# Kernel optimization log

Hardware: AMD Instinct MI355X
Metric: run time of the kernel (lower is better)

Reference implementation:

```python
import jax, jax.numpy as jnp
import numpy as np

N = 50000   # nodes
E = 800000  # edges (before self-loops)


def _gcn_conv(X, W, b, src, dst, dinv, n):
    # PyG GCNConv: out[i] = sum_j norm_ij * (X W)[j] + b, norm_ij = d_i^-1/2 d_j^-1/2
    h = X @ W                                   # [N, d_out]
    norm = dinv[src] * dinv[dst]                # [E+N]
    msg = h[src] * norm[:, None]                # gather + scale
    return jax.ops.segment_sum(msg, dst, num_segments=n) + b


def setup_inputs() -> dict:
    key = jax.random.key(0)
    k1, k2, k3, k4 = jax.random.split(key, 4)
    X = jax.random.normal(k1, (N, 128), dtype=jnp.float32)
    edge_index = jax.random.randint(k2, (2, E), 0, N, dtype=jnp.int64)
    W1 = jax.random.normal(k3, (128, 128), dtype=jnp.float32) * (1.0 / np.sqrt(128))
    b1 = jnp.zeros((128,), jnp.float32)
    W2 = jax.random.normal(k4, (128, 64), dtype=jnp.float32) * (1.0 / np.sqrt(128))
    b2 = jnp.zeros((64,), jnp.float32)
    return {"X": X, "edge_index": edge_index, "W1": W1, "b1": b1, "W2": W2, "b2": b2}


def reference(X, edge_index, W1, b1, W2, b2):
    n = X.shape[0]
    loops = jnp.arange(n, dtype=edge_index.dtype)
    src = jnp.concatenate([edge_index[0], loops])   # A + I
    dst = jnp.concatenate([edge_index[1], loops])
    deg = jax.ops.segment_sum(jnp.ones(src.shape[0], X.dtype), dst, num_segments=n)
    dinv = jnp.where(deg > 0, jax.lax.rsqrt(deg), 0.0)

    h = _gcn_conv(X, W1, b1, src, dst, dinv, n)                     # gcn1
    h = jax.nn.relu(_gcn_conv(h, W1, b1, src, dst, dinv, n))        # gcn1 again (as in source), relu
    # dropout: eval mode (identity)
    logits = _gcn_conv(h, W2, b2, src, dst, dinv, n)                # gcn2
    return jax.nn.log_softmax(logits, axis=1)
```

## Files before the change

### kernel.cpp

```cpp
#include <hip/hip_runtime.h>
#include <hip/hip_fp16.h>
#include <type_traits>

typedef _Float16 f16x8 __attribute__((ext_vector_type(8)));
typedef float    f32x4 __attribute__((ext_vector_type(4)));

__device__ inline unsigned int pack2(float a, float b) {
    __half2 h = __floats2half2_rn(a, b);
    return *(unsigned int*)&h;
}
__device__ inline float2 unpack2(unsigned int u) {
    __half2 h = *(__half2*)&u;
    return __half22float2(h);
}

#define MAXB 8192


__global__ void zero_kernel(int* __restrict__ p, int len) {
    int i = blockIdx.x * blockDim.x + threadIdx.x;
    if (i < len) p[i] = 0;
}

__global__ __launch_bounds__(256) void bucket_scatter_kernel(
    const int* __restrict__ src, const int* __restrict__ dst, int E, int nbuck,
    int* __restrict__ bcursor, unsigned int* __restrict__ staging) {
    __shared__ int hist[256];
    __shared__ int base[256];
    const int t = threadIdx.x;
    const int chunk = (E + gridDim.x - 1) / gridDim.x;
    const int e0 = blockIdx.x * chunk;
    const int e1 = min(E, e0 + chunk);
    for (int i = t; i < nbuck; i += 256) hist[i] = 0;
    __syncthreads();
    for (int e = e0 + t; e < e1; e += 256)
        atomicAdd(&hist[((unsigned)dst[e]) >> 8], 1);
    __syncthreads();
    for (int i = t; i < nbuck; i += 256) {
        int c = hist[i];
        base[i] = (c > 0) ? atomicAdd(&bcursor[i], c) : 0;
        hist[i] = 0;
    }
    __syncthreads();
    for (int e = e0 + t; e < e1; e += 256) {
        int d = dst[e];
        int b = ((unsigned)d) >> 8;
        int off = atomicAdd(&hist[b], 1);
        staging[(size_t)b * MAXB + base[b] + off] =
            (unsigned)src[e] | ((unsigned)(d & 255) << 16);
    }
}

__global__ __launch_bounds__(256) void bucket_hist_kernel(
    const unsigned int* __restrict__ staging, const int* __restrict__ bcursor,
    int n, int* __restrict__ counts, float* __restrict__ dinv) {
    __shared__ int hist[256];
    const int b = blockIdx.x, t = threadIdx.x;
    hist[t] = 0;
    __syncthreads();
    const int cnt = bcursor[b];
    const unsigned int* rec = staging + (size_t)b * MAXB;
    for (int i = t; i < cnt; i += 256) atomicAdd(&hist[(rec[i] >> 16) & 255], 1);
    __syncthreads();
    int node = (b << 8) + t;
    if (node < n) {
        int c = hist[t];
        counts[node] = c;
        dinv[node]   = rsqrtf(1.0f + (float)c);
    }
}

__global__ __launch_bounds__(256) void scan_bexcl_kernel(const int* __restrict__ bcursor,
                                                         int* __restrict__ bexcl, int nb) {
    __shared__ int s[256];
    int t = threadIdx.x;
    int v = (t < nb) ? bcursor[t] : 0;
    s[t] = v;
    __syncthreads();
    for (int off = 1; off < 256; off <<= 1) {
        int u = (t >= off) ? s[t - off] : 0;
        __syncthreads();
        s[t] += u;
        __syncthreads();
    }
    if (t < nb) bexcl[t] = s[t] - v;
}

__global__ __launch_bounds__(256) void scan_write_kernel(const int* __restrict__ counts,
                                                         const int* __restrict__ blockoff, int n,
                                                         int* __restrict__ rowptr) {
    __shared__ int s[256];
    int t = threadIdx.x;
    int i = blockIdx.x * 256 + t;
    int v = (i < n) ? counts[i] : 0;
    s[t] = v;
    __syncthreads();
    for (int off = 1; off < 256; off <<= 1) {
        int u = (t >= off) ? s[t - off] : 0;
        __syncthreads();
        s[t] += u;
        __syncthreads();
    }
    int excl = blockoff[blockIdx.x] + s[t] - v;
    if (i < n) {
        rowptr[i] = excl;
        if (i == n - 1) rowptr[n] = excl + v;
    }
}

__global__ __launch_bounds__(256) void bucket_place_kernel(
    const unsigned int* __restrict__ staging, const int* __restrict__ bcursor,
    const int* __restrict__ rowptr, int n, unsigned short* __restrict__ edges) {
    __shared__ int lcur[256];
    const int b = blockIdx.x, t = threadIdx.x;
    int node = (b << 8) + t;
    lcur[t] = rowptr[min(node, n)];
    __syncthreads();
    const int cnt = bcursor[b];
    const unsigned int* rec = staging + (size_t)b * MAXB;
    for (int i = t; i < cnt; i += 256) {
        unsigned r = rec[i];
        int dl = (r >> 16) & 255;
        int p  = atomicAdd(&lcur[dl], 1);
        edges[p] = (unsigned short)(r & 0xffffu);
    }
}

template <int DOUT, typename TIN>
__global__ __launch_bounds__(256) void gemm_mfma(const TIN* __restrict__ A,
                                                 const float* __restrict__ W,
                                                 const float* __restrict__ dinv,
                                                 __half* __restrict__ C, int n) {
    constexpr int NF = DOUT / 16;
    __shared__ __align__(16) unsigned char wlds[DOUT * 256];

    const int t = threadIdx.x;
    for (int p = t; p < 64 * DOUT; p += 256) {
        int nn = p % DOUT;
        int k  = (p / DOUT) * 2;
        float w0 = W[(size_t)k * DOUT + nn];
        float w1 = W[(size_t)(k + 1) * DOUT + nn];
        int byte = (nn * 256 + k * 2) ^ ((nn & 7) << 4);
        *(unsigned int*)(wlds + byte) = pack2(w0, w1);
    }
    __syncthreads();

    const int w  = t >> 6;
    const int l  = t & 63;
    const int m  = (blockIdx.x * 4 + w) * 16 + (l & 15);
    const int kq = l >> 4;
    const bool valid = (m < n);

    f32x4 acc[NF];
#pragma unroll
    for (int i = 0; i < NF; ++i) acc[i] = (f32x4){0.f, 0.f, 0.f, 0.f};

#pragma unroll
    for (int ks = 0; ks < 4; ++ks) {
        const int k0 = ks * 32 + kq * 8;
        f16x8 af = {0, 0, 0, 0, 0, 0, 0, 0};
        if (valid) {
            if constexpr (std::is_same<TIN, float>::value) {
                const float4 x0 = *(const float4*)&A[(size_t)m * 128 + k0];
                const float4 x1 = *(const float4*)&A[(size_t)m * 128 + k0 + 4];
                af[0] = (_Float16)x0.x; af[1] = (_Float16)x0.y;
                af[2] = (_Float16)x0.z; af[3] = (_Float16)x0.w;
                af[4] = (_Float16)x1.x; af[5] = (_Float16)x1.y;
                af[6] = (_Float16)x1.z; af[7] = (_Float16)x1.w;
            } else {
                af = *(const f16x8*)&A[(size_t)m * 128 + k0];
            }
        }
#pragma unroll
        for (int nf = 0; nf < NF; ++nf) {
            int nn = nf * 16 + (l & 15);
            int byte = (nn * 256 + k0 * 2) ^ ((nn & 7) << 4);
            f16x8 bf = *(const f16x8*)(wlds + byte);
            acc[nf] = __builtin_amdgcn_mfma_f32_16x16x32_f16(bf, af, acc[nf], 0, 0, 0);
        }
    }

    if (valid) {
        const float di = dinv[m];
#pragma unroll
        for (int nf = 0; nf < NF; ++nf) {
            uint2 o;
            o.x = pack2(di * acc[nf][0], di * acc[nf][1]);
            o.y = pack2(di * acc[nf][2], di * acc[nf][3]);
            *(uint2*)&C[(size_t)m * DOUT + nf * 16 + kq * 4] = o;
        }
    }
}

template <int DOUT, bool RELU, bool LSM, typename TOUT>
__global__ __launch_bounds__(256) void agg_kernel(const __half* __restrict__ H,
                                                  const int* __restrict__ rowptr,
                                                  const unsigned short* __restrict__ edges,
                                                  const float* __restrict__ dinv,
                                                  const float* __restrict__ bias,
                                                  TOUT* __restrict__ out, int n) {
    constexpr int LPR = DOUT / 8;
    constexpr int EPW = 64 / LPR;
    const int t    = threadIdx.x;
    const int row  = blockIdx.x * 4 + (t >> 6);
    if (row >= n) return;
    const int lane = t & 63;
    const int sub  = lane / LPR;
    const int fl   = lane % LPR;

    const uint4* Hv = (const uint4*)H;

    float a[8] = {0.f, 0.f, 0.f, 0.f, 0.f, 0.f, 0.f, 0.f};
    auto accum = [&](uint4 h) {
        float2 f;
        f = unpack2(h.x); a[0] += f.x; a[1] += f.y;
        f = unpack2(h.y); a[2] += f.x; a[3] += f.y;
        f = unpack2(h.z); a[4] += f.x; a[5] += f.y;
        f = unpack2(h.w); a[6] += f.x; a[7] += f.y;
    };

    if (sub == 0) accum(Hv[(size_t)row * LPR + fl]);

    int j        = rowptr[row] + sub;
    const int je = rowptr[row + 1];
    for (; j + EPW < je; j += 2 * EPW) {
        int s0 = edges[j];
        int s1 = edges[j + EPW];
        uint4 h0 = Hv[(size_t)s0 * LPR + fl];
        uint4 h1 = Hv[(size_t)s1 * LPR + fl];
        accum(h0);
        accum(h1);
    }
    if (j < je) accum(Hv[(size_t)edges[j] * LPR + fl]);

#pragma unroll
    for (int off = LPR; off < 64; off <<= 1) {
#pragma unroll
        for (int i = 0; i < 8; ++i) a[i] += __shfl_xor(a[i], off, 64);
    }

    const float di = dinv[row];
    const float4 b0 = ((const float4*)bias)[fl * 2];
    const float4 b1 = ((const float4*)bias)[fl * 2 + 1];
    a[0] = b0.x + di * a[0]; a[1] = b0.y + di * a[1];
    a[2] = b0.z + di * a[2]; a[3] = b0.w + di * a[3];
    a[4] = b1.x + di * a[4]; a[5] = b1.y + di * a[5];
    a[6] = b1.z + di * a[6]; a[7] = b1.w + di * a[7];

    if (RELU) {
#pragma unroll
        for (int i = 0; i < 8; ++i) a[i] = fmaxf(a[i], 0.f);
    }

    if constexpr (LSM) {
        float m8 = a[0];
#pragma unroll
        for (int i = 1; i < 8; ++i) m8 = fmaxf(m8, a[i]);
#pragma unroll
        for (int off = 1; off < LPR; off <<= 1) m8 = fmaxf(m8, __shfl_xor(m8, off, LPR));
        float s = 0.f;
#pragma unroll
        for (int i = 0; i < 8; ++i) s += expf(a[i] - m8);
#pragma unroll
        for (int off = 1; off < LPR; off <<= 1) s += __shfl_xor(s, off, LPR);
        float ls = m8 + logf(s);
        if (sub == 0) {
            float* op = (float*)out + (size_t)row * DOUT + fl * 8;
            *(float4*)op       = make_float4(a[0] - ls, a[1] - ls, a[2] - ls, a[3] - ls);
            *(float4*)(op + 4) = make_float4(a[4] - ls, a[5] - ls, a[6] - ls, a[7] - ls);
        }
    } else {
        if (sub == 0) {
            uint4 o;
            o.x = pack2(a[0], a[1]);
            o.y = pack2(a[2], a[3]);
            o.z = pack2(a[4], a[5]);
            o.w = pack2(a[6], a[7]);
            *(uint4*)&((__half*)out)[(size_t)row * DOUT + fl * 8] = o;
        }
    }
}


extern "C" void kernel_launch(void* const* d_in, const int* in_sizes, int n_in,
                              void* d_out, int out_size, void* d_ws, size_t ws_size,
                              hipStream_t stream) {
    const float* X  = (const float*)d_in[0];
    const int*   ei = (const int*)d_in[1];
    const float* W1 = (const float*)d_in[2];
    const float* b1 = (const float*)d_in[3];
    const float* W2 = (const float*)d_in[4];
    const float* b2 = (const float*)d_in[5];

    const int n = in_sizes[0] / 128;
    const int E = in_sizes[1] / 2;
    const int* src = ei;
    const int* dst = ei + E;
    const int nbuck = (n + 255) >> 8;

    char* ws = (char*)d_ws;
    size_t off = 0;
    auto alloc = [&](size_t bytes) -> void* {
        void* p = ws + off;
        off = (off + bytes + 255) & ~(size_t)255;
        return p;
    };
    float*          dinv    = (float*)alloc((size_t)n * 4);
    int*            counts  = (int*)  alloc((size_t)n * 4);
    int*            rowptr  = (int*)  alloc((size_t)(n + 1) * 4);
    int*            bcursor = (int*)  alloc((size_t)nbuck * 4);
    int*            bexcl   = (int*)  alloc((size_t)nbuck * 4);
    unsigned int*   staging = (unsigned int*)alloc((size_t)nbuck * MAXB * 4);
    unsigned short* edges   = (unsigned short*)alloc((size_t)E * 2);
    __half*         P       = (__half*)alloc((size_t)n * 128 * 2);
    __half*         Q       = (__half*)alloc((size_t)n * 128 * 2);

    const int nb = (n + 255) / 256;

    zero_kernel<<<1, 256, 0, stream>>>(bcursor, nbuck);
    bucket_scatter_kernel<<<392, 256, 0, stream>>>(src, dst, E, nbuck, bcursor, staging);
    bucket_hist_kernel<<<nbuck, 256, 0, stream>>>(staging, bcursor, n, counts, dinv);
    scan_bexcl_kernel<<<1, 256, 0, stream>>>(bcursor, bexcl, nbuck);
    scan_write_kernel<<<nb, 256, 0, stream>>>(counts, bexcl, n, rowptr);
    bucket_place_kernel<<<nbuck, 256, 0, stream>>>(staging, bcursor, rowptr, n, edges);

    const int gb = (n + 63) / 64;
    const int ab = (n + 3) / 4;

    gemm_mfma<128, float><<<gb, 256, 0, stream>>>(X, W1, dinv, P, n);
    agg_kernel<128, false, false, __half><<<ab, 256, 0, stream>>>(
        P, rowptr, edges, dinv, b1, Q, n);

    gemm_mfma<128, __half><<<gb, 256, 0, stream>>>(Q, W1, dinv, P, n);
    agg_kernel<128, true, false, __half><<<ab, 256, 0, stream>>>(
        P, rowptr, edges, dinv, b1, Q, n);

    gemm_mfma<64, __half><<<gb, 256, 0, stream>>>(Q, W2, dinv, P, n);
    agg_kernel<64, false, true, float><<<ab, 256, 0, stream>>>(
        P, rowptr, edges, dinv, b2, (float*)d_out, n);
}
```

Before: 193.7 us.

## Sort rows by degree and aggregate one row per lane group

Result: faster. 189.4 us (-2.2%).

```diff
diff --git a/kernel.cpp b/kernel.cpp
--- a/kernel.cpp
+++ b/kernel.cpp
@@ -53,10 +53,13 @@
 
 __global__ __launch_bounds__(256) void bucket_hist_kernel(
     const unsigned int* __restrict__ staging, const int* __restrict__ bcursor,
-    int n, int* __restrict__ counts, float* __restrict__ dinv) {
+    int n, int* __restrict__ counts, float* __restrict__ dinv,
+    int* __restrict__ deghist) {
     __shared__ int hist[256];
+    __shared__ int dh[256];
     const int b = blockIdx.x, t = threadIdx.x;
     hist[t] = 0;
+    dh[t] = 0;
     __syncthreads();
     const int cnt = bcursor[b];
     const unsigned int* rec = staging + (size_t)b * MAXB;
@@ -67,14 +70,17 @@
         int c = hist[t];
         counts[node] = c;
         dinv[node]   = rsqrtf(1.0f + (float)c);
-    }
-}
-
-__global__ __launch_bounds__(256) void scan_bexcl_kernel(const int* __restrict__ bcursor,
-                                                         int* __restrict__ bexcl, int nb) {
+        atomicAdd(&dh[min(c, 255)], 1);
+    }
+    __syncthreads();
+    if (dh[t] > 0) atomicAdd(&deghist[t], dh[t]);
+}
+
+__global__ __launch_bounds__(256) void scan_small_kernel(const int* __restrict__ in,
+                                                         int* __restrict__ out, int nb) {
     __shared__ int s[256];
     int t = threadIdx.x;
-    int v = (t < nb) ? bcursor[t] : 0;
+    int v = (t < nb) ? in[t] : 0;
     s[t] = v;
     __syncthreads();
     for (int off = 1; off < 256; off <<= 1) {
@@ -83,7 +89,7 @@
         s[t] += u;
         __syncthreads();
     }
-    if (t < nb) bexcl[t] = s[t] - v;
+    if (t < nb) out[t] = s[t] - v;
 }
 
 __global__ __launch_bounds__(256) void scan_write_kernel(const int* __restrict__ counts,
@@ -105,6 +111,32 @@
     if (i < n) {
         rowptr[i] = excl;
         if (i == n - 1) rowptr[n] = excl + v;
+    }
+}
+
+__global__ __launch_bounds__(256) void perm_kernel(const int* __restrict__ counts,
+                                                   int* __restrict__ degoff, int n,
+                                                   int* __restrict__ perm) {
+    __shared__ int dh[256];
+    __shared__ int dbase[256];
+    const int t = threadIdx.x;
+    const int i = blockIdx.x * 256 + t;
+    dh[t] = 0;
+    __syncthreads();
+    int c = 0;
+    const bool v = (i < n);
+    if (v) {
+        c = min(counts[i], 255);
+        atomicAdd(&dh[c], 1);
+    }
+    __syncthreads();
+    int h = dh[t];
+    dbase[t] = (h > 0) ? atomicAdd(&degoff[t], h) : 0;
+    dh[t] = 0;
+    __syncthreads();
+    if (v) {
+        int off = atomicAdd(&dh[c], 1);
+        perm[dbase[c] + off] = i;
     }
 }
 
@@ -196,21 +228,28 @@
 __global__ __launch_bounds__(256) void agg_kernel(const __half* __restrict__ H,
                                                   const int* __restrict__ rowptr,
                                                   const unsigned short* __restrict__ edges,
+                                                  const int* __restrict__ perm,
                                                   const float* __restrict__ dinv,
                                                   const float* __restrict__ bias,
                                                   TOUT* __restrict__ out, int n) {
     constexpr int LPR = DOUT / 8;
-    constexpr int EPW = 64 / LPR;
-    const int t    = threadIdx.x;
-    const int row  = blockIdx.x * 4 + (t >> 6);
-    if (row >= n) return;
-    const int lane = t & 63;
-    const int sub  = lane / LPR;
-    const int fl   = lane % LPR;
+    constexpr int RPB = 256 / LPR;
+    const int rid  = blockIdx.x * RPB + threadIdx.x / LPR;
+    const int lane = threadIdx.x % LPR;
+    if (rid >= n) return;
+    const int row = perm[rid];
 
     const uint4* Hv = (const uint4*)H;
 
-    float a[8] = {0.f, 0.f, 0.f, 0.f, 0.f, 0.f, 0.f, 0.f};
+    float a[8];
+    {
+        uint4 h = Hv[(size_t)row * LPR + lane];
+        float2 f;
+        f = unpack2(h.x); a[0] = f.x; a[1] = f.y;
+        f = unpack2(h.y); a[2] = f.x; a[3] = f.y;
+        f = unpack2(h.z); a[4] = f.x; a[5] = f.y;
+        f = unpack2(h.w); a[6] = f.x; a[7] = f.y;
+    }
     auto accum = [&](uint4 h) {
         float2 f;
         f = unpack2(h.x); a[0] += f.x; a[1] += f.y;
@@ -219,29 +258,21 @@
         f = unpack2(h.w); a[6] += f.x; a[7] += f.y;
     };
 
-    if (sub == 0) accum(Hv[(size_t)row * LPR + fl]);
-
-    int j        = rowptr[row] + sub;
+    int j        = rowptr[row];
     const int je = rowptr[row + 1];
-    for (; j + EPW < je; j += 2 * EPW) {
+    for (; j + 1 < je; j += 2) {
         int s0 = edges[j];
-        int s1 = edges[j + EPW];
-        uint4 h0 = Hv[(size_t)s0 * LPR + fl];
-        uint4 h1 = Hv[(size_t)s1 * LPR + fl];
+        int s1 = edges[j + 1];
+        uint4 h0 = Hv[(size_t)s0 * LPR + lane];
+        uint4 h1 = Hv[(size_t)s1 * LPR + lane];
         accum(h0);
         accum(h1);
     }
-    if (j < je) accum(Hv[(size_t)edges[j] * LPR + fl]);
-
-#pragma unroll
-    for (int off = LPR; off < 64; off <<= 1) {
-#pragma unroll
-        for (int i = 0; i < 8; ++i) a[i] += __shfl_xor(a[i], off, 64);
-    }
+    if (j < je) accum(Hv[(size_t)edges[j] * LPR + lane]);
 
     const float di = dinv[row];
-    const float4 b0 = ((const float4*)bias)[fl * 2];
-    const float4 b1 = ((const float4*)bias)[fl * 2 + 1];
+    const float4 b0 = ((const float4*)bias)[lane * 2];
+    const float4 b1 = ((const float4*)bias)[lane * 2 + 1];
     a[0] = b0.x + di * a[0]; a[1] = b0.y + di * a[1];
     a[2] = b0.z + di * a[2]; a[3] = b0.w + di * a[3];
     a[4] = b1.x + di * a[4]; a[5] = b1.y + di * a[5];
@@ -264,20 +295,16 @@
 #pragma unroll
         for (int off = 1; off < LPR; off <<= 1) s += __shfl_xor(s, off, LPR);
         float ls = m8 + logf(s);
-        if (sub == 0) {
-            float* op = (float*)out + (size_t)row * DOUT + fl * 8;
-            *(float4*)op       = make_float4(a[0] - ls, a[1] - ls, a[2] - ls, a[3] - ls);
-            *(float4*)(op + 4) = make_float4(a[4] - ls, a[5] - ls, a[6] - ls, a[7] - ls);
-        }
+        float* op = (float*)out + (size_t)row * DOUT + lane * 8;
+        *(float4*)op       = make_float4(a[0] - ls, a[1] - ls, a[2] - ls, a[3] - ls);
+        *(float4*)(op + 4) = make_float4(a[4] - ls, a[5] - ls, a[6] - ls, a[7] - ls);
     } else {
-        if (sub == 0) {
-            uint4 o;
-            o.x = pack2(a[0], a[1]);
-            o.y = pack2(a[2], a[3]);
-            o.z = pack2(a[4], a[5]);
-            o.w = pack2(a[6], a[7]);
-            *(uint4*)&((__half*)out)[(size_t)row * DOUT + fl * 8] = o;
-        }
+        uint4 o;
+        o.x = pack2(a[0], a[1]);
+        o.y = pack2(a[2], a[3]);
+        o.z = pack2(a[4], a[5]);
+        o.w = pack2(a[6], a[7]);
+        *(uint4*)&((__half*)out)[(size_t)row * DOUT + lane * 8] = o;
     }
 }
 
@@ -305,11 +332,15 @@
         off = (off + bytes + 255) & ~(size_t)255;
         return p;
     };
+    int*            zbuf    = (int*)  alloc((size_t)(nbuck + 256) * 4);
+    int*            bcursor = zbuf;
+    int*            deghist = zbuf + nbuck;
     float*          dinv    = (float*)alloc((size_t)n * 4);
     int*            counts  = (int*)  alloc((size_t)n * 4);
     int*            rowptr  = (int*)  alloc((size_t)(n + 1) * 4);
-    int*            bcursor = (int*)  alloc((size_t)nbuck * 4);
     int*            bexcl   = (int*)  alloc((size_t)nbuck * 4);
+    int*            degoff  = (int*)  alloc(256 * 4);
+    int*            perm    = (int*)  alloc((size_t)n * 4);
     unsigned int*   staging = (unsigned int*)alloc((size_t)nbuck * MAXB * 4);
     unsigned short* edges   = (unsigned short*)alloc((size_t)E * 2);
     __half*         P       = (__half*)alloc((size_t)n * 128 * 2);
@@ -317,25 +348,28 @@
 
     const int nb = (n + 255) / 256;
 
-    zero_kernel<<<1, 256, 0, stream>>>(bcursor, nbuck);
+    zero_kernel<<<(nbuck + 256 + 255) / 256, 256, 0, stream>>>(zbuf, nbuck + 256);
     bucket_scatter_kernel<<<392, 256, 0, stream>>>(src, dst, E, nbuck, bcursor, staging);
-    bucket_hist_kernel<<<nbuck, 256, 0, stream>>>(staging, bcursor, n, counts, dinv);
-    scan_bexcl_kernel<<<1, 256, 0, stream>>>(bcursor, bexcl, nbuck);
+    bucket_hist_kernel<<<nbuck, 256, 0, stream>>>(staging, bcursor, n, counts, dinv, deghist);
+    scan_small_kernel<<<1, 256, 0, stream>>>(bcursor, bexcl, nbuck);
+    scan_small_kernel<<<1, 256, 0, stream>>>(deghist, degoff, 256);
     scan_write_kernel<<<nb, 256, 0, stream>>>(counts, bexcl, n, rowptr);
+    perm_kernel<<<nb, 256, 0, stream>>>(counts, degoff, n, perm);
     bucket_place_kernel<<<nbuck, 256, 0, stream>>>(staging, bcursor, rowptr, n, edges);
 
     const int gb = (n + 63) / 64;
-    const int ab = (n + 3) / 4;
+    const int ab16 = (n + 15) / 16;
+    const int ab32 = (n + 31) / 32;
 
     gemm_mfma<128, float><<<gb, 256, 0, stream>>>(X, W1, dinv, P, n);
-    agg_kernel<128, false, false, __half><<<ab, 256, 0, stream>>>(
-        P, rowptr, edges, dinv, b1, Q, n);
+    agg_kernel<128, false, false, __half><<<ab16, 256, 0, stream>>>(
+        P, rowptr, edges, perm, dinv, b1, Q, n);
 
     gemm_mfma<128, __half><<<gb, 256, 0, stream>>>(Q, W1, dinv, P, n);
-    agg_kernel<128, true, false, __half><<<ab, 256, 0, stream>>>(
-        P, rowptr, edges, dinv, b1, Q, n);
+    agg_kernel<128, true, false, __half><<<ab16, 256, 0, stream>>>(
+        P, rowptr, edges, perm, dinv, b1, Q, n);
 
     gemm_mfma<64, __half><<<gb, 256, 0, stream>>>(Q, W2, dinv, P, n);
-    agg_kernel<64, false, true, float><<<ab, 256, 0, stream>>>(
-        P, rowptr, edges, dinv, b2, (float*)d_out, n);
-}
+    agg_kernel<64, false, true, float><<<ab32, 256, 0, stream>>>(
+        P, rowptr, edges, perm, dinv, b2, (float*)d_out, n);
+}
```
